# Kernel optimization log

Hardware: AMD Instinct MI355X
Metric: run time of the kernel (lower is better)

The kernel has to match this reference:

```python
import jax, jax.numpy as jnp
import numpy as np

EPS = 1e-6
K = 3
R_MIN, R_MAX = 0.5, 2.0


def setup_inputs() -> dict:
    key = jax.random.key(0)
    k0, k1, k2, k3 = jax.random.split(key, 4)
    N, C, D, H, W = 2, 32, 48, 48, 48
    T = 1 + K + 3 + 1  # num_tokens = 6
    x = jax.random.normal(k0, (N, C, D, H, W), jnp.float32)
    w_field = jax.random.normal(k1, (4 * K, C), jnp.float32) * 0.05
    b_field = jnp.zeros((4 * K,), jnp.float32)
    gates = jax.random.normal(k2, (T,), jnp.float32)
    w_mix = jax.random.normal(k3, (C, T * C), jnp.float32) * 0.02
    b_mix = jnp.zeros((C,), jnp.float32)
    return {"x": x, "w_field": w_field, "b_field": b_field, "gates": gates, "w_mix": w_mix, "b_mix": b_mix}


def _reflect(coord, size):
    # torch 'reflection' padding, align_corners=False: reflect over [-0.5, size-0.5]
    c = jnp.abs(coord + 0.5)
    m = jnp.mod(c, 2.0 * size)
    return jnp.minimum(m, 2.0 * size - m) - 0.5


def _trilinear_sample(vol, gx, gy, gz):
    # vol: (N, D, H, W, C) channels-last; gx/gy/gz: (N, K, D, H, W) normalized coords in [-1, 1]
    N, D, H, W, C = vol.shape

    def unnorm(g, size):
        return _reflect(((g + 1.0) * size - 1.0) * 0.5, float(size))

    ix, iy, iz = unnorm(gx, W), unnorm(gy, H), unnorm(gz, D)
    x0 = jnp.floor(ix); y0 = jnp.floor(iy); z0 = jnp.floor(iz)
    fx = (ix - x0)[..., None]; fy = (iy - y0)[..., None]; fz = (iz - z0)[..., None]
    x0i = jnp.clip(x0.astype(jnp.int32), 0, W - 1); x1i = jnp.clip(x0i + 1, 0, W - 1)
    y0i = jnp.clip(y0.astype(jnp.int32), 0, H - 1); y1i = jnp.clip(y0i + 1, 0, H - 1)
    z0i = jnp.clip(z0.astype(jnp.int32), 0, D - 1); z1i = jnp.clip(z0i + 1, 0, D - 1)
    n = jnp.arange(N).reshape(N, 1, 1, 1, 1)

    def g(zi, yi, xi):
        return vol[n, zi, yi, xi]  # (N, K, D, H, W, C)

    c00 = g(z0i, y0i, x0i) * (1.0 - fx) + g(z0i, y0i, x1i) * fx
    c01 = g(z0i, y1i, x0i) * (1.0 - fx) + g(z0i, y1i, x1i) * fx
    c10 = g(z1i, y0i, x0i) * (1.0 - fx) + g(z1i, y0i, x1i) * fx
    c11 = g(z1i, y1i, x0i) * (1.0 - fx) + g(z1i, y1i, x1i) * fx
    c0 = c00 * (1.0 - fy) + c01 * fy
    c1 = c10 * (1.0 - fy) + c11 * fy
    return c0 * (1.0 - fz) + c1 * fz


def reference(x, w_field, b_field, gates, w_mix, b_mix):
    N, C, D, H, W = x.shape
    # field head: 1x1x1 conv C -> 4K, split into K unit directions U and radii r
    f = jnp.einsum('ncdhw,oc->nodhw', x, w_field) + b_field[None, :, None, None, None]
    f = f.reshape(N, K, 4, D, H, W)
    v = f[:, :, :3]
    U = v / jnp.sqrt(jnp.sum(v * v, axis=2, keepdims=True) + EPS)  # (N,K,3,D,H,W)
    r_s = R_MIN + (R_MAX - R_MIN) * jax.nn.sigmoid(f[:, :, 3])     # (N,K,D,H,W)
    # base grid, align_corners=False normalized coordinates
    gz0 = ((jnp.arange(D, dtype=x.dtype) + 0.5) * 2.0 / D - 1.0)[:, None, None]
    gy0 = ((jnp.arange(H, dtype=x.dtype) + 0.5) * 2.0 / H - 1.0)[None, :, None]
    gx0 = ((jnp.arange(W, dtype=x.dtype) + 0.5) * 2.0 / W - 1.0)[None, None, :]
    ux, uy, uz = U[:, :, 0], U[:, :, 1], U[:, :, 2]
    dx = 2.0 * r_s * ux / (W + EPS)
    dy = 2.0 * r_s * uy / (H + EPS)
    dz = 2.0 * r_s * uz / (D + EPS)
    vol = jnp.transpose(x, (0, 2, 3, 4, 1))  # (N,D,H,W,C)
    xp = _trilinear_sample(vol, gx0 + dx, gy0 + dy, gz0 + dz)  # (N,K,D,H,W,C)
    xm = _trilinear_sample(vol, gx0 - dx, gy0 - dy, gz0 - dz)
    xp = jnp.transpose(xp, (0, 1, 5, 2, 3, 4))  # (N,K,C,D,H,W)
    xm = jnp.transpose(xm, (0, 1, 5, 2, 3, 4))
    a = 0.5 * (xp + xm)
    o = 0.5 * (xp - xm)
    inv_r = 1.0 / (jax.lax.stop_gradient(r_s) + EPS)  # r detached in original
    d1 = o * inv_r[:, :, None]                        # (N,K,C,D,H,W)
    G = jnp.einsum('nkadhw,nkcdhw->nacdhw', U, d1)     # (N,3,C,D,H,W)
    d2 = (xp + xm - 2.0 * x[:, None]) * (inv_r * inv_r)[:, :, None]
    L = d2.mean(axis=1)                                # (N,C,D,H,W)
    tokens = jnp.concatenate([x[:, None], a, G, L[:, None]], axis=1)  # (N,T,C,D,H,W)
    T = tokens.shape[1]
    gated = tokens * jax.nn.sigmoid(gates)[None, :, None, None, None, None]
    delta = jnp.einsum('nmdhw,om->nodhw', gated.reshape(N, T * C, D, H, W), w_mix)
    delta = delta + b_mix[None, :, None, None, None]
    return x + delta
```

## Files before the change

### kernel.cpp

```cpp
#include <hip/hip_runtime.h>
#include <math.h>

#define NB   2
#define CH   32
#define DHW  (48*48*48)
#define TT   8
#define EPSF 1e-6f

#define TILE_N   1521
#define TILE_WSTR 1522
#define GROUPS   8

#define TOK_OFF  0
#define TOK_STR  64
#define TILE_OFF 16384
#define SMEM_SZ  40736

#define WS_BT_F 0
#define WS_WF   4096
#define WS_BF   4480
#define WS_BM   4492

typedef __attribute__((ext_vector_type(8))) short short8;
typedef __attribute__((ext_vector_type(8))) _Float16 half8;
typedef __attribute__((ext_vector_type(4))) float floatx4;
typedef __attribute__((ext_vector_type(2))) _Float16 h2;

__device__ __forceinline__ h2 pkrtz(float a, float b) {
    return __builtin_bit_cast(h2, __builtin_amdgcn_cvt_pkrtz(a, b));
}
__device__ __forceinline__ unsigned pkrtz_u(float a, float b) {
    return __builtin_bit_cast(unsigned, __builtin_amdgcn_cvt_pkrtz(a, b));
}

__global__ __launch_bounds__(256) void prep_kernel(
        const float* __restrict__ w_field,
        const float* __restrict__ b_field,
        const float* __restrict__ gates,
        const float* __restrict__ w_mix,
        const float* __restrict__ b_mix,
        float* __restrict__ ws) {
    int i = blockIdx.x * 256 + threadIdx.x;
    {
        int o = i >> 8, k = i & 255, c = k >> 3, t = k & 7;
        float sg = 1.0f / (1.0f + expf(-gates[t]));
        _Float16 hv = (_Float16)(sg * w_mix[o * 256 + t * 32 + c]);
        ((unsigned short*)(ws + WS_BT_F))[o * 256 + k] = __builtin_bit_cast(unsigned short, hv);
    }
    if (i < 384) { int c = i / 12, o = i - c * 12; ws[WS_WF + i] = w_field[o * 32 + c]; }
    if (i < 12)  ws[WS_BF + i] = b_field[i];
    if (i < 32)  ws[WS_BM + i] = b_mix[i];
}

__global__ __launch_bounds__(256) void geo_main(
        const float* __restrict__ x,
        const float* __restrict__ ws,
        float* __restrict__ out) {
    __shared__ __align__(16) char smem[SMEM_SZ];
    char* tokb  = smem + TOK_OFF;
    h2*   tileP = (h2*)(smem + TILE_OFF);
    float* cbuf = (float*)smem;

    const int tid = threadIdx.x;
    const int lin = (blockIdx.x & 7) * 108 + (blockIdx.x >> 3);
    const int bx = lin % 6, by = (lin / 6) % 6, bz = (lin / 36) % 12, n = lin / 432;
    const int lx = tid & 7, ly = (tid >> 3) & 7, lz = tid >> 6;
    const int w = bx * 8 + lx, h = by * 8 + ly, d = bz * 4 + lz;
    const int xlo = bx * 8 - 2, ylo = by * 8 - 2, zlo = bz * 4 - 2;
    const int lane = tid & 63, w64 = tid & 192;

    const float* xn = x + (size_t)n * CH * DHW;

    int goff[6];
#pragma unroll
    for (int i = 0; i < 6; ++i) {
        int e  = tid + i * 256;
        int ee = (e < TILE_N) ? e : 0;
        int tz = ee / 169; int r0 = ee - tz * 169;
        int ty = r0 / 13;  int tx = r0 - ty * 13;
        int zg = min(max(zlo + tz, 0), 47);
        int yg = min(max(ylo + ty, 0), 47);
        int xg = min(max(xlo + tx, 0), 47);
        goff[i] = (zg * 48 + yg) * 48 + xg;
    }

    const int pos = (d * 48 + h) * 48 + w;
    float f[12];
#pragma unroll
    for (int o = 0; o < 12; ++o) f[o] = ws[WS_BF + o];
    for (int c = 0; c < CH; ++c) {
        float xv = xn[c * DHW + pos];
        const float* wf = ws + WS_WF + c * 12;
#pragma unroll
        for (int o = 0; o < 12; ++o) f[o] = fmaf(wf[o], xv, f[o]);
    }

    h2 fx2[6], fy2[6], fz2[6];
    int a00[6], a01[6], a10[6], a11[6];
    float uxk[3], uyk[3], uzk[3], irk[3], ir2k[3];
    const float cscale = 48.0f / (48.0f + EPSF);
#pragma unroll
    for (int k = 0; k < 3; ++k) {
        float vx = f[4*k], vy = f[4*k+1], vz = f[4*k+2], s = f[4*k+3];
        float inv = 1.0f / sqrtf(vx*vx + vy*vy + vz*vz + EPSF);
        float ux = vx * inv, uy = vy * inv, uz = vz * inv;
        float r  = 0.5f + 1.5f / (1.0f + expf(-s));
        uxk[k] = ux; uyk[k] = uy; uzk[k] = uz;
        float ir = 1.0f / (r + EPSF); irk[k] = ir; ir2k[k] = ir * ir;
#pragma unroll
        for (int sgn = 0; sgn < 2; ++sgn) {
            int   si = 2 * k + sgn;
            float sf = sgn ? -1.0f : 1.0f;
            float txr = (float)w + sf * r * ux * cscale;
            float tyr = (float)h + sf * r * uy * cscale;
            float tzr = (float)d + sf * r * uz * cscale;
            float cx = fabsf(txr + 0.5f); float ix = fminf(cx, 96.0f - cx) - 0.5f;
            float cy = fabsf(tyr + 0.5f); float iy = fminf(cy, 96.0f - cy) - 0.5f;
            float cz = fabsf(tzr + 0.5f); float iz = fminf(cz, 96.0f - cz) - 0.5f;
            float x0f = floorf(ix), y0f = floorf(iy), z0f = floorf(iz);
            float fx = ix - x0f, fy = iy - y0f, fz = iz - z0f;
            int x0 = min(max((int)x0f, 0), 47); int x1 = min(x0 + 1, 47);
            int y0 = min(max((int)y0f, 0), 47); int y1 = min(y0 + 1, 47);
            int z0 = min(max((int)z0f, 0), 47); int z1 = min(z0 + 1, 47);
            float fxe = (x1 == x0) ? 0.0f : fx;
            _Float16 hx = (_Float16)fxe, hy = (_Float16)fy, hz = (_Float16)fz;
            fx2[si] = (h2){hx, hx}; fy2[si] = (h2){hy, hy}; fz2[si] = (h2){hz, hz};
            int lz0 = z0 - zlo, lz1 = z1 - zlo;
            int ly0 = y0 - ylo, ly1 = y1 - ylo;
            int lx0 = x0 - xlo;
            a00[si] = (lz0 * 13 + ly0) * 13 + lx0;
            a01[si] = (lz0 * 13 + ly1) * 13 + lx0;
            a10[si] = (lz1 * 13 + ly0) * 13 + lx0;
            a11[si] = (lz1 * 13 + ly1) * 13 + lx0;
        }
    }

    if (tid == 0) {
#pragma unroll
        for (int p = 0; p < 4; ++p) tileP[p * TILE_WSTR + TILE_N] = (h2){0, 0};
    }
    {
        float ld[24];
#pragma unroll
        for (int cg = 0; cg < 4; ++cg) {
            const float* xc = xn + cg * DHW;
#pragma unroll
            for (int i = 0; i < 6; ++i) ld[cg * 6 + i] = xc[goff[i]];
        }
#pragma unroll
        for (int p = 0; p < 2; ++p)
#pragma unroll
            for (int i = 0; i < 6; ++i) {
                int e = tid + i * 256;
                if (e < TILE_N)
                    tileP[p * TILE_WSTR + e] = pkrtz(ld[(2*p) * 6 + i], ld[(2*p+1) * 6 + i]);
            }
    }
    __syncthreads();

    floatx4 acc[4][2];
#pragma unroll
    for (int mt = 0; mt < 4; ++mt)
#pragma unroll
        for (int nt = 0; nt < 2; ++nt) acc[mt][nt] = (floatx4){0.f, 0.f, 0.f, 0.f};

    const int self = ((lz + 2) * 13 + (ly + 2)) * 13 + (lx + 2);
    const unsigned short* bt = (const unsigned short*)(ws + WS_BT_F);
    const int tokq = (tid >> 3) & 3;
    const int qm = lane >> 4, nlo = lane & 15;

    short8 bc0 = *(const short8*)(bt + (nlo * 256 + qm * 8));
    short8 bc1 = *(const short8*)(bt + ((nlo + 16) * 256 + qm * 8));

    for (int g = 0; g < GROUPS; ++g) {
        const int rb = (g & 1) * 2;
        const int wb = 2 - rb;
        float nld[24];
        short8 bn0 = bc0, bn1 = bc1;
        if (g < GROUPS - 1) {
            const float* xg = xn + (g + 1) * 4 * DHW;
#pragma unroll
            for (int cg = 0; cg < 4; ++cg) {
                const float* xc = xg + cg * DHW;
#pragma unroll
                for (int i = 0; i < 6; ++i) nld[cg * 6 + i] = xc[goff[i]];
            }
            bn0 = *(const short8*)(bt + (nlo * 256 + (g + 1) * 32 + qm * 8));
            bn1 = *(const short8*)(bt + ((nlo + 16) * 256 + (g + 1) * 32 + qm * 8));
        }
#pragma unroll
        for (int p = 0; p < 2; ++p) {
            const h2* tb = tileP + (rb + p) * TILE_WSTR;
            h2 s2 = tb[self];
            h2 v2[6];
#pragma unroll
            for (int si = 0; si < 6; ++si) {
                int b00 = a00[si], b01 = a01[si], b10 = a10[si], b11 = a11[si];
                h2 v000 = tb[b00], v001 = tb[b00 + 1];
                h2 v010 = tb[b01], v011 = tb[b01 + 1];
                h2 v100 = tb[b10], v101 = tb[b10 + 1];
                h2 v110 = tb[b11], v111 = tb[b11 + 1];
                h2 c00 = v000 + fx2[si] * (v001 - v000);
                h2 c01 = v010 + fx2[si] * (v011 - v010);
                h2 c10 = v100 + fx2[si] * (v101 - v100);
                h2 c11 = v110 + fx2[si] * (v111 - v110);
                h2 c0  = c00 + fy2[si] * (c01 - c00);
                h2 c1  = c10 + fy2[si] * (c11 - c10);
                v2[si] = c0 + fz2[si] * (c1 - c0);
            }
#pragma unroll
            for (int sub = 0; sub < 2; ++sub) {
                float xv = sub ? (float)s2.y : (float)s2.x;
                float val[6];
#pragma unroll
                for (int si = 0; si < 6; ++si)
                    val[si] = sub ? (float)v2[si].y : (float)v2[si].x;
                float t1, t2, t3, gx, gy, gz, l;
                {
                    float sp, sm, d1;
                    sp = val[0]; sm = val[1]; t1 = 0.5f * (sp + sm);
                    d1 = 0.5f * (sp - sm) * irk[0];
                    gx = uxk[0] * d1; gy = uyk[0] * d1; gz = uzk[0] * d1;
                    l  = (sp + sm - 2.0f * xv) * ir2k[0];
                    sp = val[2]; sm = val[3]; t2 = 0.5f * (sp + sm);
                    d1 = 0.5f * (sp - sm) * irk[1];
                    gx = fmaf(uxk[1], d1, gx); gy = fmaf(uyk[1], d1, gy); gz = fmaf(uzk[1], d1, gz);
                    l  = fmaf(sp + sm - 2.0f * xv, ir2k[1], l);
                    sp = val[4]; sm = val[5]; t3 = 0.5f * (sp + sm);
                    d1 = 0.5f * (sp - sm) * irk[2];
                    gx = fmaf(uxk[2], d1, gx); gy = fmaf(uyk[2], d1, gy); gz = fmaf(uzk[2], d1, gz);
                    l  = fmaf(sp + sm - 2.0f * xv, ir2k[2], l);
                }
                uint4 tw;
                tw.x = pkrtz_u(xv, t1);
                tw.y = pkrtz_u(t2, t3);
                tw.z = pkrtz_u(gx, gy);
                tw.w = pkrtz_u(gz, l * (1.0f / 3.0f));
                int cg = 2 * p + sub;
                int qe = cg ^ tokq;
                *(uint4*)(tokb + tid * TOK_STR + qe * 16) = tw;
            }
        }
        {
            half8 hb0 = __builtin_bit_cast(half8, bc0);
            half8 hb1 = __builtin_bit_cast(half8, bc1);
#pragma unroll
            for (int mt = 0; mt < 4; ++mt) {
                int row = w64 + mt * 16 + nlo;
                int qe  = qm ^ ((row >> 3) & 3);
                half8 a = __builtin_bit_cast(half8,
                          *(const short8*)(tokb + row * TOK_STR + qe * 16));
                acc[mt][0] = __builtin_amdgcn_mfma_f32_16x16x32_f16(a, hb0, acc[mt][0], 0, 0, 0);
                acc[mt][1] = __builtin_amdgcn_mfma_f32_16x16x32_f16(a, hb1, acc[mt][1], 0, 0, 0);
            }
        }
        bc0 = bn0; bc1 = bn1;

        if (g < GROUPS - 1) {
#pragma unroll
            for (int p = 0; p < 2; ++p)
#pragma unroll
                for (int i = 0; i < 6; ++i) {
                    int e = tid + i * 256;
                    if (e < TILE_N)
                        tileP[(wb + p) * TILE_WSTR + e] = pkrtz(nld[(2*p) * 6 + i], nld[(2*p+1) * 6 + i]);
                }
        }
        __syncthreads();
    }

    {
#pragma unroll
        for (int mt = 0; mt < 4; ++mt)
#pragma unroll
            for (int nt = 0; nt < 2; ++nt)
#pragma unroll
                for (int r = 0; r < 4; ++r) {
                    int v = w64 + mt * 16 + qm * 4 + r;
                    int col = nt * 16 + nlo;
                    cbuf[v * 36 + (col ^ (v & 31))] = acc[mt][nt][r];
                }
    }
    __syncthreads();

    const float* dr = cbuf + tid * 36;
    float* on = out + (size_t)n * CH * DHW;
#pragma unroll
    for (int o = 0; o < 32; ++o)
        __builtin_nontemporal_store(
            xn[o * DHW + pos] + dr[o ^ (tid & 31)] + ws[WS_BM + o],
            on + o * DHW + pos);
}

extern "C" void kernel_launch(void* const* d_in, const int* in_sizes, int n_in,
                              void* d_out, int out_size, void* d_ws, size_t ws_size,
                              hipStream_t stream) {
    const float *x = (const float*)d_in[0], *w_field = (const float*)d_in[1],
                *b_field = (const float*)d_in[2], *gates = (const float*)d_in[3],
                *w_mix = (const float*)d_in[4], *b_mix = (const float*)d_in[5];
    for (int i = 0; i < n_in; ++i) {
        switch (in_sizes[i]) {
            case NB * CH * DHW: x       = (const float*)d_in[i]; break;
            case 12 * CH:       w_field = (const float*)d_in[i]; break;
            case 12:            b_field = (const float*)d_in[i]; break;
            case TT:            gates   = (const float*)d_in[i]; break;
            case CH * TT * CH:  w_mix   = (const float*)d_in[i]; break;
            case CH:            b_mix   = (const float*)d_in[i]; break;
            default: break;
        }
    }
    float* ws = (float*)d_ws;
    prep_kernel<<<32, 256, 0, stream>>>(w_field, b_field, gates, w_mix, b_mix, ws);
    geo_main<<<864, 256, 0, stream>>>(x, ws, (float*)d_out);
}
```

Measured before the change: 160.2 us.

## Split each voxel's channel pairs across two thread halves in 512-thread blocks

Doubles the block to 512 threads, with each half handling one channel pair of every 4-channel group for the same 256 voxels. The halo tile layout becomes interleaved 8-byte entries per voxel, so both halves share the same address computations. The MFMA work is split across 8 waves at 2 M-tiles each, and the output stores are split by channel halves. This halves per-thread sampling and loading work to raise parallelism, at the cost of an extra __syncthreads per group and possible register or field-head duplication, since both halves recompute the field head.

```diff
diff --git a/kernel.cpp b/kernel.cpp
--- a/kernel.cpp
+++ b/kernel.cpp
@@ -9,12 +9,13 @@
 
 #define TILE_N   1521
 #define TILE_WSTR 1522
+#define TILE_BYTES (TILE_WSTR*8)
 #define GROUPS   8
 
 #define TOK_OFF  0
 #define TOK_STR  64
 #define TILE_OFF 16384
-#define SMEM_SZ  40736
+#define SMEM_SZ  (16384 + 2*TILE_BYTES)
 
 #define WS_BT_F 0
 #define WS_WF   4096
@@ -52,29 +53,31 @@
     if (i < 32)  ws[WS_BM + i] = b_mix[i];
 }
 
-__global__ __launch_bounds__(256) void geo_main(
+__global__ __launch_bounds__(512) void geo_main(
         const float* __restrict__ x,
         const float* __restrict__ ws,
         float* __restrict__ out) {
     __shared__ __align__(16) char smem[SMEM_SZ];
     char* tokb  = smem + TOK_OFF;
-    h2*   tileP = (h2*)(smem + TILE_OFF);
+    char* tileb = smem + TILE_OFF;
     float* cbuf = (float*)smem;
 
-    const int tid = threadIdx.x;
+    const int tid  = threadIdx.x;
+    const int v    = tid & 255;
+    const int half = tid >> 8;
     const int lin = (blockIdx.x & 7) * 108 + (blockIdx.x >> 3);
     const int bx = lin % 6, by = (lin / 6) % 6, bz = (lin / 36) % 12, n = lin / 432;
-    const int lx = tid & 7, ly = (tid >> 3) & 7, lz = tid >> 6;
+    const int lx = v & 7, ly = (v >> 3) & 7, lz = v >> 6;
     const int w = bx * 8 + lx, h = by * 8 + ly, d = bz * 4 + lz;
     const int xlo = bx * 8 - 2, ylo = by * 8 - 2, zlo = bz * 4 - 2;
-    const int lane = tid & 63, w64 = tid & 192;
+    const int lane = tid & 63, wv = tid >> 6;
 
     const float* xn = x + (size_t)n * CH * DHW;
 
     int goff[6];
 #pragma unroll
     for (int i = 0; i < 6; ++i) {
-        int e  = tid + i * 256;
+        int e  = v + i * 256;
         int ee = (e < TILE_N) ? e : 0;
         int tz = ee / 169; int r0 = ee - tz * 169;
         int ty = r0 / 13;  int tx = r0 - ty * 13;
@@ -128,125 +131,117 @@
             int lz0 = z0 - zlo, lz1 = z1 - zlo;
             int ly0 = y0 - ylo, ly1 = y1 - ylo;
             int lx0 = x0 - xlo;
-            a00[si] = (lz0 * 13 + ly0) * 13 + lx0;
-            a01[si] = (lz0 * 13 + ly1) * 13 + lx0;
-            a10[si] = (lz1 * 13 + ly0) * 13 + lx0;
-            a11[si] = (lz1 * 13 + ly1) * 13 + lx0;
+            a00[si] = (((lz0 * 13 + ly0) * 13 + lx0)) * 8;
+            a01[si] = (((lz0 * 13 + ly1) * 13 + lx0)) * 8;
+            a10[si] = (((lz1 * 13 + ly0) * 13 + lx0)) * 8;
+            a11[si] = (((lz1 * 13 + ly1) * 13 + lx0)) * 8;
         }
     }
 
     if (tid == 0) {
-#pragma unroll
-        for (int p = 0; p < 4; ++p) tileP[p * TILE_WSTR + TILE_N] = (h2){0, 0};
+        *(float*)(tileb + TILE_N * 8) = 0.f; *(float*)(tileb + TILE_N * 8 + 4) = 0.f;
+        *(float*)(tileb + TILE_BYTES + TILE_N * 8) = 0.f;
+        *(float*)(tileb + TILE_BYTES + TILE_N * 8 + 4) = 0.f;
     }
     {
-        float ld[24];
-#pragma unroll
-        for (int cg = 0; cg < 4; ++cg) {
-            const float* xc = xn + cg * DHW;
-#pragma unroll
-            for (int i = 0; i < 6; ++i) ld[cg * 6 + i] = xc[goff[i]];
-        }
-#pragma unroll
-        for (int p = 0; p < 2; ++p)
-#pragma unroll
-            for (int i = 0; i < 6; ++i) {
-                int e = tid + i * 256;
-                if (e < TILE_N)
-                    tileP[p * TILE_WSTR + e] = pkrtz(ld[(2*p) * 6 + i], ld[(2*p+1) * 6 + i]);
-            }
+        const float* xc = xn + (2 * half) * DHW;
+        float ld[12];
+#pragma unroll
+        for (int i = 0; i < 6; ++i) { ld[i] = xc[goff[i]]; ld[6 + i] = xc[DHW + goff[i]]; }
+#pragma unroll
+        for (int i = 0; i < 6; ++i) {
+            int e = v + i * 256;
+            if (e < TILE_N)
+                *(h2*)(tileb + e * 8 + half * 4) = pkrtz(ld[i], ld[6 + i]);
+        }
     }
     __syncthreads();
 
-    floatx4 acc[4][2];
-#pragma unroll
-    for (int mt = 0; mt < 4; ++mt)
+    floatx4 acc[2][2];
+#pragma unroll
+    for (int mt = 0; mt < 2; ++mt)
 #pragma unroll
         for (int nt = 0; nt < 2; ++nt) acc[mt][nt] = (floatx4){0.f, 0.f, 0.f, 0.f};
 
-    const int self = ((lz + 2) * 13 + (ly + 2)) * 13 + (lx + 2);
+    const int selfb = (((lz + 2) * 13 + (ly + 2)) * 13 + (lx + 2)) * 8;
     const unsigned short* bt = (const unsigned short*)(ws + WS_BT_F);
-    const int tokq = (tid >> 3) & 3;
+    const int tokq = (v >> 3) & 3;
     const int qm = lane >> 4, nlo = lane & 15;
 
     short8 bc0 = *(const short8*)(bt + (nlo * 256 + qm * 8));
     short8 bc1 = *(const short8*)(bt + ((nlo + 16) * 256 + qm * 8));
 
     for (int g = 0; g < GROUPS; ++g) {
-        const int rb = (g & 1) * 2;
-        const int wb = 2 - rb;
-        float nld[24];
+        const int rb = (g & 1);
+        const int wb = rb ^ 1;
+        float nld[12];
         short8 bn0 = bc0, bn1 = bc1;
         if (g < GROUPS - 1) {
-            const float* xg = xn + (g + 1) * 4 * DHW;
-#pragma unroll
-            for (int cg = 0; cg < 4; ++cg) {
-                const float* xc = xg + cg * DHW;
-#pragma unroll
-                for (int i = 0; i < 6; ++i) nld[cg * 6 + i] = xc[goff[i]];
-            }
+            const float* xc = xn + ((g + 1) * 4 + 2 * half) * DHW;
+#pragma unroll
+            for (int i = 0; i < 6; ++i) { nld[i] = xc[goff[i]]; nld[6 + i] = xc[DHW + goff[i]]; }
             bn0 = *(const short8*)(bt + (nlo * 256 + (g + 1) * 32 + qm * 8));
             bn1 = *(const short8*)(bt + ((nlo + 16) * 256 + (g + 1) * 32 + qm * 8));
         }
-#pragma unroll
-        for (int p = 0; p < 2; ++p) {
-            const h2* tb = tileP + (rb + p) * TILE_WSTR;
-            h2 s2 = tb[self];
-            h2 v2[6];
-#pragma unroll
-            for (int si = 0; si < 6; ++si) {
-                int b00 = a00[si], b01 = a01[si], b10 = a10[si], b11 = a11[si];
-                h2 v000 = tb[b00], v001 = tb[b00 + 1];
-                h2 v010 = tb[b01], v011 = tb[b01 + 1];
-                h2 v100 = tb[b10], v101 = tb[b10 + 1];
-                h2 v110 = tb[b11], v111 = tb[b11 + 1];
-                h2 c00 = v000 + fx2[si] * (v001 - v000);
-                h2 c01 = v010 + fx2[si] * (v011 - v010);
-                h2 c10 = v100 + fx2[si] * (v101 - v100);
-                h2 c11 = v110 + fx2[si] * (v111 - v110);
-                h2 c0  = c00 + fy2[si] * (c01 - c00);
-                h2 c1  = c10 + fy2[si] * (c11 - c10);
-                v2[si] = c0 + fz2[si] * (c1 - c0);
+        const char* tb = tileb + rb * TILE_BYTES + half * 4;
+        h2 s2 = *(const h2*)(tb + selfb);
+        h2 v2[6];
+#pragma unroll
+        for (int si = 0; si < 6; ++si) {
+            int b00 = a00[si], b01 = a01[si], b10 = a10[si], b11 = a11[si];
+            h2 v000 = *(const h2*)(tb + b00), v001 = *(const h2*)(tb + b00 + 8);
+            h2 v010 = *(const h2*)(tb + b01), v011 = *(const h2*)(tb + b01 + 8);
+            h2 v100 = *(const h2*)(tb + b10), v101 = *(const h2*)(tb + b10 + 8);
+            h2 v110 = *(const h2*)(tb + b11), v111 = *(const h2*)(tb + b11 + 8);
+            h2 fx = fx2[si], fy = fy2[si], fz = fz2[si];
+            h2 c00 = v000 + fx * (v001 - v000);
+            h2 c01 = v010 + fx * (v011 - v010);
+            h2 c10 = v100 + fx * (v101 - v100);
+            h2 c11 = v110 + fx * (v111 - v110);
+            h2 c0  = c00 + fy * (c01 - c00);
+            h2 c1  = c10 + fy * (c11 - c10);
+            v2[si] = c0 + fz * (c1 - c0);
+        }
+#pragma unroll
+        for (int sub = 0; sub < 2; ++sub) {
+            float xv = sub ? (float)s2.y : (float)s2.x;
+            float val[6];
+#pragma unroll
+            for (int si = 0; si < 6; ++si)
+                val[si] = sub ? (float)v2[si].y : (float)v2[si].x;
+            float t1, t2, t3, gx, gy, gz, l;
+            {
+                float sp, sm, d1;
+                sp = val[0]; sm = val[1]; t1 = 0.5f * (sp + sm);
+                d1 = 0.5f * (sp - sm) * irk[0];
+                gx = uxk[0] * d1; gy = uyk[0] * d1; gz = uzk[0] * d1;
+                l  = (sp + sm - 2.0f * xv) * ir2k[0];
+                sp = val[2]; sm = val[3]; t2 = 0.5f * (sp + sm);
+                d1 = 0.5f * (sp - sm) * irk[1];
+                gx = fmaf(uxk[1], d1, gx); gy = fmaf(uyk[1], d1, gy); gz = fmaf(uzk[1], d1, gz);
+                l  = fmaf(sp + sm - 2.0f * xv, ir2k[1], l);
+                sp = val[4]; sm = val[5]; t3 = 0.5f * (sp + sm);
+                d1 = 0.5f * (sp - sm) * irk[2];
+                gx = fmaf(uxk[2], d1, gx); gy = fmaf(uyk[2], d1, gy); gz = fmaf(uzk[2], d1, gz);
+                l  = fmaf(sp + sm - 2.0f * xv, ir2k[2], l);
             }
-#pragma unroll
-            for (int sub = 0; sub < 2; ++sub) {
-                float xv = sub ? (float)s2.y : (float)s2.x;
-                float val[6];
-#pragma unroll
-                for (int si = 0; si < 6; ++si)
-                    val[si] = sub ? (float)v2[si].y : (float)v2[si].x;
-                float t1, t2, t3, gx, gy, gz, l;
-                {
-                    float sp, sm, d1;
-                    sp = val[0]; sm = val[1]; t1 = 0.5f * (sp + sm);
-                    d1 = 0.5f * (sp - sm) * irk[0];
-                    gx = uxk[0] * d1; gy = uyk[0] * d1; gz = uzk[0] * d1;
-                    l  = (sp + sm - 2.0f * xv) * ir2k[0];
-                    sp = val[2]; sm = val[3]; t2 = 0.5f * (sp + sm);
-                    d1 = 0.5f * (sp - sm) * irk[1];
-                    gx = fmaf(uxk[1], d1, gx); gy = fmaf(uyk[1], d1, gy); gz = fmaf(uzk[1], d1, gz);
-                    l  = fmaf(sp + sm - 2.0f * xv, ir2k[1], l);
-                    sp = val[4]; sm = val[5]; t3 = 0.5f * (sp + sm);
-                    d1 = 0.5f * (sp - sm) * irk[2];
-                    gx = fmaf(uxk[2], d1, gx); gy = fmaf(uyk[2], d1, gy); gz = fmaf(uzk[2], d1, gz);
-                    l  = fmaf(sp + sm - 2.0f * xv, ir2k[2], l);
-                }
-                uint4 tw;
-                tw.x = pkrtz_u(xv, t1);
-                tw.y = pkrtz_u(t2, t3);
-                tw.z = pkrtz_u(gx, gy);
-                tw.w = pkrtz_u(gz, l * (1.0f / 3.0f));
-                int cg = 2 * p + sub;
-                int qe = cg ^ tokq;
-                *(uint4*)(tokb + tid * TOK_STR + qe * 16) = tw;
-            }
-        }
+            uint4 tw;
+            tw.x = pkrtz_u(xv, t1);
+            tw.y = pkrtz_u(t2, t3);
+            tw.z = pkrtz_u(gx, gy);
+            tw.w = pkrtz_u(gz, l * (1.0f / 3.0f));
+            int cg = 2 * half + sub;
+            int qe = cg ^ tokq;
+            *(uint4*)(tokb + v * TOK_STR + qe * 16) = tw;
+        }
+        __syncthreads();
+
         {
             half8 hb0 = __builtin_bit_cast(half8, bc0);
             half8 hb1 = __builtin_bit_cast(half8, bc1);
 #pragma unroll
-            for (int mt = 0; mt < 4; ++mt) {
-                int row = w64 + mt * 16 + nlo;
+            for (int mt = 0; mt < 2; ++mt) {
+                int row = wv * 32 + mt * 16 + nlo;
                 int qe  = qm ^ ((row >> 3) & 3);
                 half8 a = __builtin_bit_cast(half8,
                           *(const short8*)(tokb + row * TOK_STR + qe * 16));
@@ -258,38 +253,38 @@
 
         if (g < GROUPS - 1) {
 #pragma unroll
-            for (int p = 0; p < 2; ++p)
-#pragma unroll
-                for (int i = 0; i < 6; ++i) {
-                    int e = tid + i * 256;
-                    if (e < TILE_N)
-                        tileP[(wb + p) * TILE_WSTR + e] = pkrtz(nld[(2*p) * 6 + i], nld[(2*p+1) * 6 + i]);
+            for (int i = 0; i < 6; ++i) {
+                int e = v + i * 256;
+                if (e < TILE_N)
+                    *(h2*)(tileb + wb * TILE_BYTES + e * 8 + half * 4) = pkrtz(nld[i], nld[6 + i]);
+            }
+        }
+        __syncthreads();
+    }
+
+    {
+#pragma unroll
+        for (int mt = 0; mt < 2; ++mt)
+#pragma unroll
+            for (int nt = 0; nt < 2; ++nt)
+#pragma unroll
+                for (int r = 0; r < 4; ++r) {
+                    int vr = wv * 32 + mt * 16 + qm * 4 + r;
+                    int col = nt * 16 + nlo;
+                    cbuf[vr * 36 + (col ^ (vr & 31))] = acc[mt][nt][r];
                 }
-        }
-        __syncthreads();
-    }
-
-    {
-#pragma unroll
-        for (int mt = 0; mt < 4; ++mt)
-#pragma unroll
-            for (int nt = 0; nt < 2; ++nt)
-#pragma unroll
-                for (int r = 0; r < 4; ++r) {
-                    int v = w64 + mt * 16 + qm * 4 + r;
-                    int col = nt * 16 + nlo;
-                    cbuf[v * 36 + (col ^ (v & 31))] = acc[mt][nt][r];
-                }
     }
     __syncthreads();
 
-    const float* dr = cbuf + tid * 36;
+    const float* dr = cbuf + v * 36;
     float* on = out + (size_t)n * CH * DHW;
 #pragma unroll
-    for (int o = 0; o < 32; ++o)
+    for (int o = 0; o < 16; ++o) {
+        int oo = half * 16 + o;
         __builtin_nontemporal_store(
-            xn[o * DHW + pos] + dr[o ^ (tid & 31)] + ws[WS_BM + o],
-            on + o * DHW + pos);
+            xn[oo * DHW + pos] + dr[oo ^ (v & 31)] + ws[WS_BM + oo],
+            on + oo * DHW + pos);
+    }
 }
 
 extern "C" void kernel_launch(void* const* d_in, const int* in_sizes, int n_in,
@@ -311,5 +306,5 @@
     }
     float* ws = (float*)d_ws;
     prep_kernel<<<32, 256, 0, stream>>>(w_field, b_field, gates, w_mix, b_mix, ws);
-    geo_main<<<864, 256, 0, stream>>>(x, ws, (float*)d_out);
-}
+    geo_main<<<864, 512, 0, stream>>>(x, ws, (float*)d_out);
+}
```

Result: slower. 196.5 us (+22.6%).
